# Kernel tuning notes

Hardware: AMD Instinct MI355X
Metric: run time of the kernel (lower is better)

## Reference

```python
import jax, jax.numpy as jnp
import numpy as np

N = 100000          # nodes
E = 1600000         # edges (avg degree 16)
DIN = 64
DOUT = 64
EXPERTS = 3
GATE_C = 4
TEMP = 101.0        # batch=0 < decay_lim: 100 - 0 + final_temperature(1.0)


def setup_inputs() -> dict:
    key = jax.random.key(0)
    ks = jax.random.split(key, 6)
    x = jax.random.normal(ks[0], (N, DIN), dtype=jnp.float32)
    edge_index = jax.random.randint(ks[1], (2, E), 0, N, dtype=jnp.int32)
    gate_features = jax.random.normal(ks[2], (N, GATE_C), dtype=jnp.float32)
    # per-expert GCN linear weights/bias (PyG GCNConv: lin then bias)
    W = jax.random.normal(ks[3], (EXPERTS, DIN, DOUT), dtype=jnp.float32) / np.sqrt(DIN).astype(np.float32)
    b = jnp.zeros((EXPERTS, DOUT), dtype=jnp.float32)
    # gating nn.Linear(gate_channels, experts, bias=False); stored as [GATE_C, EXPERTS] so y = gf @ Wg
    Wg = jax.random.normal(ks[4], (GATE_C, EXPERTS), dtype=jnp.float32) / np.sqrt(GATE_C).astype(np.float32)
    return {"x": x, "edge_index": edge_index, "gate_features": gate_features,
            "W": W, "b": b, "Wg": Wg}


def reference(x, edge_index, gate_features, W, b, Wg):
    n = x.shape[0]
    # --- GCN normalization with self-loops (PyG GCNConv defaults) ---
    loops = jnp.arange(n, dtype=edge_index.dtype)
    rows = jnp.concatenate([edge_index[0], loops])   # source nodes, [E+N]
    cols = jnp.concatenate([edge_index[1], loops])   # target nodes, [E+N]
    deg = jax.ops.segment_sum(jnp.ones(rows.shape, dtype=x.dtype), cols, num_segments=n)
    dinv = jnp.where(deg > 0, jax.lax.rsqrt(deg), 0.0)
    norm = dinv[rows] * dinv[cols]                   # [E+N]

    # --- gating network (softmax with decayed temperature) ---
    gate = jax.nn.softmax((gate_features @ Wg) / jnp.asarray(TEMP, x.dtype), axis=-1)  # [N, EXPERTS]

    # --- experts: GCN conv -> ReLU -> gate-weighted accumulation ---
    out = jnp.zeros((n, W.shape[-1]), dtype=x.dtype)
    for i in range(W.shape[0]):                      # small fixed expert count
        xw = x @ W[i]                                # [N, DOUT]
        msg = xw[rows] * norm[:, None]               # gather + scale, [E+N, DOUT]
        agg = jax.ops.segment_sum(msg, cols, num_segments=n) + b[i]
        out = out + gate[:, i:i + 1] * jax.nn.relu(agg)
    return out
```

## Files before the change

### kernel.cpp

```cpp
#include <hip/hip_runtime.h>
#include <hip/hip_bf16.h>

#define NN 100000
#define NE 1600000
#define NT 6250

#define NBUCK  511
#define BRANGE 196
#define CAPB   3584
#define CHUNK  4096
#define NCH    391

typedef __attribute__((ext_vector_type(8))) short bf16x8;
typedef __attribute__((ext_vector_type(4))) float f32x4;

__device__ inline float2 bf16x2_unpack(unsigned v) {
    float2 r;
    r.x = __uint_as_float(v << 16);
    r.y = __uint_as_float(v & 0xffff0000u);
    return r;
}
__device__ inline unsigned bf16x2_pack(float a, float b) {
    __hip_bfloat162 h2(__float2bfloat16(a), __float2bfloat16(b));
    unsigned u;
    __builtin_memcpy(&u, &h2, 4);
    return u;
}

__global__ __launch_bounds__(512) void bin_kernel(const int* __restrict__ rows,
                                                  const int* __restrict__ cols,
                                                  int* __restrict__ cur,
                                                  unsigned* __restrict__ eb) {
    __shared__ int hist[512];
    __shared__ int excl[512];
    __shared__ int lcur[512];
    __shared__ int gbase[512];
    __shared__ unsigned staged[CHUNK];
    __shared__ unsigned short bktarr[CHUNK];
    int t = threadIdx.x;
    int base = blockIdx.x * CHUNK;
    int cnt = min(CHUNK, NE - base);

    if (t < 512) hist[t] = 0;
    __syncthreads();

    int cbuf[CHUNK / 512];
    int rbuf[CHUNK / 512];
    #pragma unroll
    for (int k = 0; k < CHUNK / 512; k++) {
        int i = k * 512 + t;
        int c = (i < cnt) ? cols[base + i] : -1;
        int r = (i < cnt) ? rows[base + i] : 0;
        cbuf[k] = c;
        rbuf[k] = r;
        if (c >= 0) atomicAdd(&hist[(unsigned)c / BRANGE], 1);
    }
    __syncthreads();

    if (t < 64) {
        int carry = 0;
        #pragma unroll
        for (int k = 0; k < 8; k++) {
            int e = k * 64 + t;
            int h = hist[e];
            int inc = h;
            #pragma unroll
            for (int off = 1; off < 64; off <<= 1) {
                int v = __shfl_up(inc, off);
                if (t >= off) inc += v;
            }
            int ex = carry + inc - h;
            excl[e] = ex;
            lcur[e] = ex;
            carry += __shfl(inc, 63);
        }
    }
    __syncthreads();

    if (t < 512) {
        int h = hist[t];
        gbase[t] = h ? atomicAdd(cur + t * 16, h) : 0;
    }
    __syncthreads();

    #pragma unroll
    for (int k = 0; k < CHUNK / 512; k++) {
        int c = cbuf[k];
        if (c >= 0) {
            int bkt = (unsigned)c / BRANGE;
            int lp = atomicAdd(&lcur[bkt], 1);
            staged[lp] = ((unsigned)(c - bkt * BRANGE) << 24) | (unsigned)rbuf[k];
            bktarr[lp] = (unsigned short)bkt;
        }
    }
    __syncthreads();

    #pragma unroll
    for (int k = 0; k < CHUNK / 512; k++) {
        int i = k * 512 + t;
        if (i < cnt) {
            int bkt = bktarr[i];
            int pos = gbase[bkt] + (i - excl[bkt]);
            if (pos < CAPB) eb[(size_t)bkt * CAPB + pos] = staged[i];
        }
    }
}

__global__ __launch_bounds__(1024) void sortn_kernel(const int* __restrict__ cur,
                                                     const unsigned* __restrict__ eb,
                                                     int* __restrict__ srcs2,
                                                     int2* __restrict__ nsd) {
    __shared__ unsigned recs[CAPB];
    __shared__ unsigned srcl[CAPB];
    __shared__ int hist[256];
    __shared__ int lcur[256];
    int b = blockIdx.x, t = threadIdx.x;
    if (t < 256) hist[t] = 0;
    __syncthreads();
    int cnt = min(cur[b * 16], CAPB);
    const unsigned* seg = eb + (size_t)b * CAPB;
    for (int i = t; i < cnt; i += 1024) {
        unsigned r = seg[i];
        recs[i] = r;
        atomicAdd(&hist[r >> 24], 1);
    }
    __syncthreads();
    if (t < 64) {
        int e = t * 4;
        int h0 = hist[e], h1 = hist[e + 1], h2 = hist[e + 2], h3 = hist[e + 3];
        int lsum = h0 + h1 + h2 + h3;
        int inc = lsum;
        #pragma unroll
        for (int off = 1; off < 64; off <<= 1) {
            int v = __shfl_up(inc, off);
            if (t >= off) inc += v;
        }
        int ex = inc - lsum;
        int e0 = ex, e1 = ex + h0, e2 = e1 + h1, e3 = e2 + h2;
        lcur[e] = e0; lcur[e + 1] = e1; lcur[e + 2] = e2; lcur[e + 3] = e3;
        int n = b * BRANGE + e;
        if (e     < BRANGE && n     < NN) nsd[n]     = make_int2(e0, h0);
        if (e + 1 < BRANGE && n + 1 < NN) nsd[n + 1] = make_int2(e1, h1);
        if (e + 2 < BRANGE && n + 2 < NN) nsd[n + 2] = make_int2(e2, h2);
        if (e + 3 < BRANGE && n + 3 < NN) nsd[n + 3] = make_int2(e3, h3);
    }
    __syncthreads();
    for (int i = t; i < cnt; i += 1024) {
        unsigned r = recs[i];
        int p = atomicAdd(&lcur[r >> 24], 1);
        srcl[p] = r & 0xFFFFFFu;
    }
    __syncthreads();
    for (int i = t; i < cnt; i += 1024)
        srcs2[(size_t)b * CAPB + i] = (int)srcl[i];
}

__global__ __launch_bounds__(256) void xscale_kernel(const float* __restrict__ x,
                                                     const int2* __restrict__ nsd,
                                                     unsigned* __restrict__ xs) {
    int i = blockIdx.x * 256 + threadIdx.x;
    int n = i >> 5;
    int d = (i & 31) * 2;
    float2 v = *(const float2*)(x + (size_t)n * 64 + d);
    float dv = rsqrtf((float)(nsd[n].y + 1));
    xs[i] = bf16x2_pack(v.x * dv, v.y * dv);
}

__global__ __launch_bounds__(256) void gather_kernel(const int* __restrict__ srcs2,
                                                     const int2* __restrict__ nsd,
                                                     const unsigned* __restrict__ xs,
                                                     unsigned* __restrict__ hbu) {
    int lane = threadIdx.x & 63;
    int wave = threadIdx.x >> 6;
    int g  = lane >> 4;
    int gl = lane & 15;
    int gb = g << 4;

    int n = blockIdx.x * 16 + wave * 4 + g;
    int2 sd = nsd[n];
    int deg = sd.y;
    int bkt = (unsigned)n / BRANGE;
    const int* seg = srcs2 + (size_t)bkt * CAPB + sd.x;
    const uint2* xsv = (const uint2*)xs;

    float4 acc = make_float4(0.f, 0.f, 0.f, 0.f);
    for (int base = 0; base < deg; base += 16) {
        int idx = 0;
        if (base + gl < deg) idx = seg[base + gl];
        int s0 = __shfl(idx, gb);
        uint2 v[16];
        #pragma unroll
        for (int j = 0; j < 16; j++) {
            int s = __shfl(idx, gb + j);
            s = (base + j < deg) ? s : s0;
            v[j] = xsv[(size_t)s * 16 + gl];
        }
        #pragma unroll
        for (int j = 0; j < 16; j++) {
            if (base + j < deg) {
                float2 f0 = bf16x2_unpack(v[j].x);
                float2 f1 = bf16x2_unpack(v[j].y);
                acc.x += f0.x; acc.y += f0.y;
                acc.z += f1.x; acc.w += f1.y;
            }
        }
    }
    uint2 svu = xsv[(size_t)n * 16 + gl];
    float2 sv0 = bf16x2_unpack(svu.x);
    float2 sv1 = bf16x2_unpack(svu.y);
    float dn = rsqrtf((float)(deg + 1));
    uint2 o;
    o.x = bf16x2_pack((acc.x + sv0.x) * dn, (acc.y + sv0.y) * dn);
    o.y = bf16x2_pack((acc.z + sv1.x) * dn, (acc.w + sv1.y) * dn);
    ((uint2*)hbu)[(size_t)n * 16 + gl] = o;
}

__global__ void wpack_kernel(const float* __restrict__ W, __hip_bfloat16* __restrict__ Bp) {
    int idx = blockIdx.x * 256 + threadIdx.x;
    if (idx >= 12288) return;
    int j    = idx & 7;
    int lane = (idx >> 3) & 63;
    int rest = idx >> 9;
    int t    = rest % 12;
    int kh   = rest / 12;
    int k    = kh * 32 + (lane >> 4) * 8 + j;
    int col  = t * 16 + (lane & 15);
    int i    = col >> 6;
    int d    = col & 63;
    Bp[idx] = __float2bfloat16(W[(i * 64 + k) * 64 + d]);
}

__global__ __launch_bounds__(256) void mfma_kernel(const __hip_bfloat16* __restrict__ hb,
                                                   const short* __restrict__ Bp,
                                                   const float* __restrict__ b,
                                                   const float* __restrict__ gf,
                                                   const float* __restrict__ Wg,
                                                   float* __restrict__ out) {
    int wave = threadIdx.x >> 6;
    int lane = threadIdx.x & 63;
    int tile = blockIdx.x * 4 + wave;
    if (tile >= NT) return;
    int n0 = tile * 16;
    int m = lane & 15, quad = lane >> 4;

    const short* hrow = (const short*)hb + ((size_t)(n0 + m)) * 64 + quad * 8;
    bf16x8 a0 = *(const bf16x8*)(hrow);
    bf16x8 a1 = *(const bf16x8*)(hrow + 32);

    f32x4 acc[12];
    #pragma unroll
    for (int t = 0; t < 12; t++) acc[t] = (f32x4)(0.0f);

    #pragma unroll
    for (int kh = 0; kh < 2; kh++) {
        bf16x8 a = kh ? a1 : a0;
        #pragma unroll
        for (int t = 0; t < 12; t++) {
            bf16x8 bf = *(const bf16x8*)(Bp + ((size_t)((kh * 12 + t) * 64 + lane)) * 8);
            acc[t] = __builtin_amdgcn_mfma_f32_16x16x32_bf16(a, bf, acc[t], 0, 0, 0);
        }
    }

    float wg[12];
    #pragma unroll
    for (int k = 0; k < 12; k++) wg[k] = Wg[k];

    #pragma unroll
    for (int reg = 0; reg < 4; reg++) {
        int n = n0 + quad * 4 + reg;
        float4 g = ((const float4*)gf)[n];
        float l0 = (g.x*wg[0] + g.y*wg[3] + g.z*wg[6] + g.w*wg[9])  * (1.0f/101.0f);
        float l1 = (g.x*wg[1] + g.y*wg[4] + g.z*wg[7] + g.w*wg[10]) * (1.0f/101.0f);
        float l2 = (g.x*wg[2] + g.y*wg[5] + g.z*wg[8] + g.w*wg[11]) * (1.0f/101.0f);
        float mx = fmaxf(l0, fmaxf(l1, l2));
        float e0 = __expf(l0 - mx), e1 = __expf(l1 - mx), e2 = __expf(l2 - mx);
        float inv = 1.0f / (e0 + e1 + e2);
        float g0 = e0 * inv, g1 = e1 * inv, g2 = e2 * inv;
        #pragma unroll
        for (int dpos = 0; dpos < 4; dpos++) {
            int d = dpos * 16 + m;
            float v0 = acc[0*4 + dpos][reg] + b[0*64 + d];
            float v1 = acc[1*4 + dpos][reg] + b[1*64 + d];
            float v2 = acc[2*4 + dpos][reg] + b[2*64 + d];
            float o = g0 * fmaxf(v0, 0.f) + g1 * fmaxf(v1, 0.f) + g2 * fmaxf(v2, 0.f);
            out[(size_t)n * 64 + d] = o;
        }
    }
}

extern "C" void kernel_launch(void* const* d_in, const int* in_sizes, int n_in,
                              void* d_out, int out_size, void* d_ws, size_t ws_size,
                              hipStream_t stream) {
    const float* x  = (const float*)d_in[0];
    const int*   ei = (const int*)d_in[1];
    const float* gf = (const float*)d_in[2];
    const float* W  = (const float*)d_in[3];
    const float* b  = (const float*)d_in[4];
    const float* Wg = (const float*)d_in[5];
    float* out = (float*)d_out;
    const int* rows = ei;
    const int* cols = ei + NE;

    char* ws = (char*)d_ws;
    size_t off = 0;
    auto alloc = [&](size_t bytes) {
        char* p = ws + off;
        off = (off + bytes + 255) & ~(size_t)255;
        return p;
    };
    int*            cur   = (int*)alloc(512 * 16 * 4);
    unsigned*       eb    = (unsigned*)alloc((size_t)NBUCK * CAPB * 4);
    int*            srcs2 = (int*)alloc((size_t)NBUCK * CAPB * 4);
    int2*           nsd   = (int2*)alloc((size_t)NN * 8);
    unsigned*       xs    = (unsigned*)alloc((size_t)NN * 32 * 4);
    unsigned*       hbu   = (unsigned*)alloc((size_t)NN * 32 * 4);
    __hip_bfloat16* Bp    = (__hip_bfloat16*)alloc(12288 * 2);

    hipMemsetAsync(cur, 0, 512 * 16 * 4, stream);

    bin_kernel<<<NCH, 512, 0, stream>>>(rows, cols, cur, eb);
    sortn_kernel<<<NBUCK, 1024, 0, stream>>>(cur, eb, srcs2, nsd);
    xscale_kernel<<<NN * 32 / 256, 256, 0, stream>>>(x, nsd, xs);
    wpack_kernel<<<48, 256, 0, stream>>>(W, Bp);
    gather_kernel<<<NN / 16, 256, 0, stream>>>(srcs2, nsd, xs, hbu);
    mfma_kernel<<<(NT + 3) / 4, 256, 0, stream>>>((const __hip_bfloat16*)hbu,
                                                  (const short*)Bp, b, gf, Wg, out);
}
```

Baseline: 169.3 us.

## Fuse neighbor gather and expert MFMA into one kernel via LDS tile

```diff
diff --git a/kernel.cpp b/kernel.cpp
--- a/kernel.cpp
+++ b/kernel.cpp
@@ -166,55 +166,6 @@
     xs[i] = bf16x2_pack(v.x * dv, v.y * dv);
 }
 
-__global__ __launch_bounds__(256) void gather_kernel(const int* __restrict__ srcs2,
-                                                     const int2* __restrict__ nsd,
-                                                     const unsigned* __restrict__ xs,
-                                                     unsigned* __restrict__ hbu) {
-    int lane = threadIdx.x & 63;
-    int wave = threadIdx.x >> 6;
-    int g  = lane >> 4;
-    int gl = lane & 15;
-    int gb = g << 4;
-
-    int n = blockIdx.x * 16 + wave * 4 + g;
-    int2 sd = nsd[n];
-    int deg = sd.y;
-    int bkt = (unsigned)n / BRANGE;
-    const int* seg = srcs2 + (size_t)bkt * CAPB + sd.x;
-    const uint2* xsv = (const uint2*)xs;
-
-    float4 acc = make_float4(0.f, 0.f, 0.f, 0.f);
-    for (int base = 0; base < deg; base += 16) {
-        int idx = 0;
-        if (base + gl < deg) idx = seg[base + gl];
-        int s0 = __shfl(idx, gb);
-        uint2 v[16];
-        #pragma unroll
-        for (int j = 0; j < 16; j++) {
-            int s = __shfl(idx, gb + j);
-            s = (base + j < deg) ? s : s0;
-            v[j] = xsv[(size_t)s * 16 + gl];
-        }
-        #pragma unroll
-        for (int j = 0; j < 16; j++) {
-            if (base + j < deg) {
-                float2 f0 = bf16x2_unpack(v[j].x);
-                float2 f1 = bf16x2_unpack(v[j].y);
-                acc.x += f0.x; acc.y += f0.y;
-                acc.z += f1.x; acc.w += f1.y;
-            }
-        }
-    }
-    uint2 svu = xsv[(size_t)n * 16 + gl];
-    float2 sv0 = bf16x2_unpack(svu.x);
-    float2 sv1 = bf16x2_unpack(svu.y);
-    float dn = rsqrtf((float)(deg + 1));
-    uint2 o;
-    o.x = bf16x2_pack((acc.x + sv0.x) * dn, (acc.y + sv0.y) * dn);
-    o.y = bf16x2_pack((acc.z + sv1.x) * dn, (acc.w + sv1.y) * dn);
-    ((uint2*)hbu)[(size_t)n * 16 + gl] = o;
-}
-
 __global__ void wpack_kernel(const float* __restrict__ W, __hip_bfloat16* __restrict__ Bp) {
     int idx = blockIdx.x * 256 + threadIdx.x;
     if (idx >= 12288) return;
@@ -230,34 +181,78 @@
     Bp[idx] = __float2bfloat16(W[(i * 64 + k) * 64 + d]);
 }
 
-__global__ __launch_bounds__(256) void mfma_kernel(const __hip_bfloat16* __restrict__ hb,
-                                                   const short* __restrict__ Bp,
-                                                   const float* __restrict__ b,
-                                                   const float* __restrict__ gf,
-                                                   const float* __restrict__ Wg,
-                                                   float* __restrict__ out) {
+__global__ __launch_bounds__(256) void gmm_kernel(const int* __restrict__ srcs2,
+                                                  const int2* __restrict__ nsd,
+                                                  const unsigned* __restrict__ xs,
+                                                  const short* __restrict__ Bp,
+                                                  const float* __restrict__ bias,
+                                                  const float* __restrict__ gf,
+                                                  const float* __restrict__ Wg,
+                                                  float* __restrict__ out) {
+    __shared__ unsigned atile[16][32];
+    int lane = threadIdx.x & 63;
     int wave = threadIdx.x >> 6;
-    int lane = threadIdx.x & 63;
-    int tile = blockIdx.x * 4 + wave;
-    if (tile >= NT) return;
-    int n0 = tile * 16;
+    int g  = lane >> 4;
+    int gl = lane & 15;
+    int gb = g << 4;
+    int n0 = blockIdx.x * 16;
+
+    int nl = wave * 4 + g;
+    int n = n0 + nl;
+    int2 sd = nsd[n];
+    int deg = sd.y;
+    int bkt = (unsigned)n / BRANGE;
+    const int* seg = srcs2 + (size_t)bkt * CAPB + sd.x;
+    const uint2* xsv = (const uint2*)xs;
+
+    float4 acc = make_float4(0.f, 0.f, 0.f, 0.f);
+    for (int base = 0; base < deg; base += 16) {
+        int idx = 0;
+        if (base + gl < deg) idx = seg[base + gl];
+        int s0 = __shfl(idx, gb);
+        uint2 v[16];
+        #pragma unroll
+        for (int j = 0; j < 16; j++) {
+            int s = __shfl(idx, gb + j);
+            s = (base + j < deg) ? s : s0;
+            v[j] = xsv[(size_t)s * 16 + gl];
+        }
+        #pragma unroll
+        for (int j = 0; j < 16; j++) {
+            if (base + j < deg) {
+                float2 f0 = bf16x2_unpack(v[j].x);
+                float2 f1 = bf16x2_unpack(v[j].y);
+                acc.x += f0.x; acc.y += f0.y;
+                acc.z += f1.x; acc.w += f1.y;
+            }
+        }
+    }
+    uint2 svu = xsv[(size_t)n * 16 + gl];
+    float2 sv0 = bf16x2_unpack(svu.x);
+    float2 sv1 = bf16x2_unpack(svu.y);
+    float dn = rsqrtf((float)(deg + 1));
+    uint2 o;
+    o.x = bf16x2_pack((acc.x + sv0.x) * dn, (acc.y + sv0.y) * dn);
+    o.y = bf16x2_pack((acc.z + sv1.x) * dn, (acc.w + sv1.y) * dn);
+    ((uint2*)atile[nl])[gl] = o;
+    __syncthreads();
+
     int m = lane & 15, quad = lane >> 4;
-
-    const short* hrow = (const short*)hb + ((size_t)(n0 + m)) * 64 + quad * 8;
-    bf16x8 a0 = *(const bf16x8*)(hrow);
-    bf16x8 a1 = *(const bf16x8*)(hrow + 32);
-
-    f32x4 acc[12];
-    #pragma unroll
-    for (int t = 0; t < 12; t++) acc[t] = (f32x4)(0.0f);
-
+    int dpos = wave;
+    const bf16x8* arow = (const bf16x8*)atile[m];
+    bf16x8 a0 = arow[quad];
+    bf16x8 a1 = arow[quad + 4];
+
+    f32x4 ce[3];
+    #pragma unroll
+    for (int e = 0; e < 3; e++) ce[e] = (f32x4)(0.0f);
     #pragma unroll
     for (int kh = 0; kh < 2; kh++) {
         bf16x8 a = kh ? a1 : a0;
         #pragma unroll
-        for (int t = 0; t < 12; t++) {
-            bf16x8 bf = *(const bf16x8*)(Bp + ((size_t)((kh * 12 + t) * 64 + lane)) * 8);
-            acc[t] = __builtin_amdgcn_mfma_f32_16x16x32_bf16(a, bf, acc[t], 0, 0, 0);
+        for (int e = 0; e < 3; e++) {
+            bf16x8 bf = *(const bf16x8*)(Bp + ((size_t)((kh * 12 + e * 4 + dpos) * 64 + lane)) * 8);
+            ce[e] = __builtin_amdgcn_mfma_f32_16x16x32_bf16(a, bf, ce[e], 0, 0, 0);
         }
     }
 
@@ -265,26 +260,23 @@
     #pragma unroll
     for (int k = 0; k < 12; k++) wg[k] = Wg[k];
 
+    int d = dpos * 16 + m;
+    float b0 = bias[0 * 64 + d], b1 = bias[1 * 64 + d], b2 = bias[2 * 64 + d];
     #pragma unroll
     for (int reg = 0; reg < 4; reg++) {
-        int n = n0 + quad * 4 + reg;
-        float4 g = ((const float4*)gf)[n];
-        float l0 = (g.x*wg[0] + g.y*wg[3] + g.z*wg[6] + g.w*wg[9])  * (1.0f/101.0f);
-        float l1 = (g.x*wg[1] + g.y*wg[4] + g.z*wg[7] + g.w*wg[10]) * (1.0f/101.0f);
-        float l2 = (g.x*wg[2] + g.y*wg[5] + g.z*wg[8] + g.w*wg[11]) * (1.0f/101.0f);
+        int nn = n0 + quad * 4 + reg;
+        float4 gv = ((const float4*)gf)[nn];
+        float l0 = (gv.x*wg[0] + gv.y*wg[3] + gv.z*wg[6] + gv.w*wg[9])  * (1.0f/101.0f);
+        float l1 = (gv.x*wg[1] + gv.y*wg[4] + gv.z*wg[7] + gv.w*wg[10]) * (1.0f/101.0f);
+        float l2 = (gv.x*wg[2] + gv.y*wg[5] + gv.z*wg[8] + gv.w*wg[11]) * (1.0f/101.0f);
         float mx = fmaxf(l0, fmaxf(l1, l2));
         float e0 = __expf(l0 - mx), e1 = __expf(l1 - mx), e2 = __expf(l2 - mx);
         float inv = 1.0f / (e0 + e1 + e2);
-        float g0 = e0 * inv, g1 = e1 * inv, g2 = e2 * inv;
-        #pragma unroll
-        for (int dpos = 0; dpos < 4; dpos++) {
-            int d = dpos * 16 + m;
-            float v0 = acc[0*4 + dpos][reg] + b[0*64 + d];
-            float v1 = acc[1*4 + dpos][reg] + b[1*64 + d];
-            float v2 = acc[2*4 + dpos][reg] + b[2*64 + d];
-            float o = g0 * fmaxf(v0, 0.f) + g1 * fmaxf(v1, 0.f) + g2 * fmaxf(v2, 0.f);
-            out[(size_t)n * 64 + d] = o;
-        }
+        float v0 = ce[0][reg] + b0;
+        float v1 = ce[1][reg] + b1;
+        float v2 = ce[2][reg] + b2;
+        float ov = (e0 * fmaxf(v0, 0.f) + e1 * fmaxf(v1, 0.f) + e2 * fmaxf(v2, 0.f)) * inv;
+        out[(size_t)nn * 64 + d] = ov;
     }
 }
 
@@ -313,7 +305,6 @@
     int*            srcs2 = (int*)alloc((size_t)NBUCK * CAPB * 4);
     int2*           nsd   = (int2*)alloc((size_t)NN * 8);
     unsigned*       xs    = (unsigned*)alloc((size_t)NN * 32 * 4);
-    unsigned*       hbu   = (unsigned*)alloc((size_t)NN * 32 * 4);
     __hip_bfloat16* Bp    = (__hip_bfloat16*)alloc(12288 * 2);
 
     hipMemsetAsync(cur, 0, 512 * 16 * 4, stream);
@@ -322,7 +313,5 @@
     sortn_kernel<<<NBUCK, 1024, 0, stream>>>(cur, eb, srcs2, nsd);
     xscale_kernel<<<NN * 32 / 256, 256, 0, stream>>>(x, nsd, xs);
     wpack_kernel<<<48, 256, 0, stream>>>(W, Bp);
-    gather_kernel<<<NN / 16, 256, 0, stream>>>(srcs2, nsd, xs, hbu);
-    mfma_kernel<<<(NT + 3) / 4, 256, 0, stream>>>((const __hip_bfloat16*)hbu,
-                                                  (const short*)Bp, b, gf, Wg, out);
-}
+    gmm_kernel<<<NT, 256, 0, stream>>>(srcs2, nsd, xs, (const short*)Bp, b, gf, Wg, out);
+}
```

Measured after the change: 165.6 us. 2.2% less time.
